# Optimization experiments

Measured on AMD Instinct MI355X. Metric: run time of the kernel, lower is better.

The kernel has to match this reference:

```python
import jax, jax.numpy as jnp
import numpy as np

B, S, DM = 2, 2048, 1024
H, HD = 16, 64  # heads, head_dims = dims // heads
SCALE = HD ** -0.5


def softmax_one(x):
    # softmax with +1 in the denominator: exp(x_i) / (1 + sum_j exp(x_j))
    # stable form: shift by m = max(max(x), 0)
    m = jnp.maximum(jnp.max(x, axis=-1, keepdims=True), 0.0)
    e = jnp.exp(x - m)
    return e / (jnp.exp(-m) + jnp.sum(e, axis=-1, keepdims=True))


def setup_inputs() -> dict:
    key = jax.random.key(0)
    ks = jax.random.split(key, 11)
    init = lambda k, shape, fan_in: jax.random.uniform(k, shape, jnp.float32, -1.0, 1.0) * (fan_in ** -0.5)
    return {
        "query": jax.random.normal(ks[0], (B, S, DM), jnp.float32),
        "key": jax.random.normal(ks[1], (B, S, DM), jnp.float32),
        "value": jax.random.normal(ks[2], (B, S, DM), jnp.float32),
        "Wq": init(ks[3], (H * HD, DM), DM), "bq": init(ks[4], (H * HD,), DM),
        "Wk": init(ks[5], (H * HD, DM), DM), "bk": init(ks[6], (H * HD,), DM),
        "Wv": init(ks[7], (H * HD, DM), DM), "bv": init(ks[8], (H * HD,), DM),
        "Wo": init(ks[9], (DM, H * HD), H * HD), "bo": init(ks[10], (DM,), H * HD),
    }


def _proj(x, W, b):
    # [B,S,DM] -> [B,H,S,HD]
    y = x @ W.T + b
    return y.reshape(B, S, H, HD).transpose(0, 2, 1, 3)


def reference(query, key, value, Wq, bq, Wk, bk, Wv, bv, Wo, bo):
    Q = _proj(query, Wq, bq)
    K = _proj(key, Wk, bk)
    V = _proj(value, Wv, bv)
    scores = jnp.einsum("bhqd,bhkd->bhqk", Q, K) * SCALE  # [B,H,S,S]
    attn = softmax_one(scores)
    out = jnp.einsum("bhqk,bhkd->bhqd", attn, V)  # [B,H,S,HD]
    out = out.transpose(0, 2, 1, 3).reshape(B, S, H * HD)
    return out @ Wo.T + bo
```

## Files before the change

### kernel.cpp

```cpp
#include <hip/hip_runtime.h>

#define B_ 2
#define S_ 2048
#define DM_ 1024
#define H_ 16
#define HD_ 64
#define QSCALE_ 0.18033688011112042f

typedef __bf16 bf16;
typedef __attribute__((ext_vector_type(4))) __bf16 bf16x4;
typedef __attribute__((ext_vector_type(8))) __bf16 bf16x8;
typedef __attribute__((ext_vector_type(4))) float f32x4;

#define MFMA16(a, b, c) __builtin_amdgcn_mfma_f32_16x16x32_bf16((a), (b), (c), 0, 0, 0)
#define EXP2(x) __builtin_amdgcn_exp2f(x)

__device__ __forceinline__ void async16(const bf16* g, bf16* l) {
  __builtin_amdgcn_global_load_lds(
      (const __attribute__((address_space(1))) void*)g,
      (__attribute__((address_space(3))) void*)l, 16, 0, 0);
}

__global__ __launch_bounds__(256) void convert_kernel(
    const float* __restrict__ q, const float* __restrict__ k,
    const float* __restrict__ v, const float* __restrict__ wq,
    const float* __restrict__ wk, const float* __restrict__ wv,
    const float* __restrict__ wo, bf16* __restrict__ dst) {
  size_t idx = ((size_t)blockIdx.x * 256 + threadIdx.x) * 8;
  const float* src;
  size_t off;
  if (idx < 4194304) { src = q; off = idx; }
  else if (idx < 8388608) { src = k; off = idx - 4194304; }
  else if (idx < 12582912) { src = v; off = idx - 8388608; }
  else if (idx < 13631488) { src = wq; off = idx - 12582912; }
  else if (idx < 14680064) { src = wk; off = idx - 13631488; }
  else if (idx < 15728640) { src = wv; off = idx - 14680064; }
  else { src = wo; off = idx - 15728640; }
  float4 a = *(const float4*)(src + off);
  float4 b = *(const float4*)(src + off + 4);
  bf16x8 o;
  o[0] = (bf16)a.x; o[1] = (bf16)a.y; o[2] = (bf16)a.z; o[3] = (bf16)a.w;
  o[4] = (bf16)b.x; o[5] = (bf16)b.y; o[6] = (bf16)b.z; o[7] = (bf16)b.w;
  *(bf16x8*)(dst + idx) = o;
}

template <int MODE>
__device__ __forceinline__ void gemm_body(const bf16* A, const bf16* W,
                                          const float* bias, bf16* C,
                                          float scale) {
  constexpr int K = 1024;
  __shared__ __align__(16) bf16 smem[128 * 136];
  bf16* As = smem;
  bf16* Bs = smem + 128 * 64;
  const int t = threadIdx.x;
  const int lane = t & 63, wave = t >> 6;
  const int quad = lane >> 4, l16 = lane & 15;
  const int m0 = blockIdx.y * 128, n0 = blockIdx.x * 128;
  const int wm = (wave >> 1) * 64, wn = (wave & 1) * 64;

  const f32x4 zero = {0.f, 0.f, 0.f, 0.f};
  f32x4 acc[4][4];
  for (int i = 0; i < 4; i++)
    for (int j = 0; j < 4; j++) acc[i][j] = zero;

  for (int k0 = 0; k0 < K; k0 += 64) {
    for (int i = 0; i < 4; ++i) {
      int c = i * 256 + t;
      int row = c >> 3, g = c & 7;
      int off = k0 + ((g ^ (row & 7)) * 8);
      async16(A + (size_t)(m0 + row) * K + off, As + c * 8);
      async16(W + (size_t)(n0 + row) * K + off, Bs + c * 8);
    }
    __syncthreads();

    for (int ks = 0; ks < 2; ks++) {
      bf16x8 af[4], bfr[4];
      for (int mb = 0; mb < 4; mb++) {
        int ra = wm + mb * 16 + l16;
        af[mb] = *(const bf16x8*)(As + ra * 64 + ((ks * 4 + quad) ^ (ra & 7)) * 8);
        int rb = wn + mb * 16 + l16;
        bfr[mb] = *(const bf16x8*)(Bs + rb * 64 + ((ks * 4 + quad) ^ (rb & 7)) * 8);
      }
      for (int mb = 0; mb < 4; mb++)
        for (int nb = 0; nb < 4; nb++)
          acc[mb][nb] = MFMA16(af[mb], bfr[nb], acc[mb][nb]);
    }
    __syncthreads();
  }

  if constexpr (MODE == 2) {
    bf16* Ct = smem;
    for (int nb = 0; nb < 4; nb++) {
      int cl = wn + nb * 16 + l16;
      float bv = bias[n0 + cl] * scale;
      for (int mb = 0; mb < 4; mb++) {
        int rowb = wm + mb * 16 + quad * 4;
        bf16x4 v;
        for (int r = 0; r < 4; r++)
          v[r] = (bf16)(acc[mb][nb][r] * scale + bv);
        *(bf16x4*)(Ct + cl * 136 + rowb) = v;
      }
    }
    __syncthreads();
    int c = t >> 1, half = t & 1;
    int colg = n0 + c;
    int hh = colg >> 6, dd = colg & 63;
    int bb = m0 >> 11, s0 = m0 & (S_ - 1);
    bf16* dst = C + (((size_t)(bb * H_ + hh)) * HD_ + dd) * S_ + s0 + half * 64;
    const bf16* srcr = Ct + c * 136 + half * 64;
    for (int j = 0; j < 8; ++j)
      *(bf16x8*)(dst + j * 8) = *(const bf16x8*)(srcr + j * 8);
  } else {
    for (int nb = 0; nb < 4; nb++) {
      int col = n0 + wn + nb * 16 + l16;
      float bv = bias[col] * scale;
      for (int mb = 0; mb < 4; mb++) {
        int rowb = m0 + wm + mb * 16 + quad * 4;
        for (int r = 0; r < 4; r++) {
          int row = rowb + r;
          float o = acc[mb][nb][r] * scale + bv;
          int bb = row >> 11, s = row & (S_ - 1);
          int h = col >> 6, d = col & 63;
          C[(((size_t)(bb * H_ + h)) * S_ + s) * HD_ + d] = (bf16)o;
        }
      }
    }
  }
}

__global__ __launch_bounds__(256, 4) void qkv_proj_kernel(
    const bf16* Xc, const float* bq, const float* bk, const float* bv,
    bf16* Qo, bf16* Ko, bf16* Vo) {
  int z = blockIdx.z;
  const bf16* A = Xc + (size_t)z * 4194304;
  const bf16* W = Xc + 12582912 + (size_t)z * 1048576;
  if (z == 0)
    gemm_body<1>(A, W, bq, Qo, QSCALE_);
  else if (z == 1)
    gemm_body<1>(A, W, bk, Ko, 1.0f);
  else
    gemm_body<2>(A, W, bv, Vo, 1.0f);
}

__global__ __launch_bounds__(256) void out_proj_kernel(const bf16* A,
                                                       const bf16* W,
                                                       const float* bias,
                                                       float* C) {
  constexpr int K = 1024, N = 1024;
  __shared__ __align__(16) bf16 As[64 * 64];
  __shared__ __align__(16) bf16 Bs[128 * 64];
  const int t = threadIdx.x;
  const int lane = t & 63, wave = t >> 6;
  const int quad = lane >> 4, l16 = lane & 15;
  const int m0 = blockIdx.y * 64, n0 = blockIdx.x * 128;

  const f32x4 zero = {0.f, 0.f, 0.f, 0.f};
  f32x4 acc[8];
  for (int i = 0; i < 8; i++) acc[i] = zero;

  for (int k0 = 0; k0 < K; k0 += 64) {
    for (int i = 0; i < 2; ++i) {
      int c = i * 256 + t;
      int row = c >> 3, g = c & 7;
      async16(A + (size_t)(m0 + row) * K + k0 + ((g ^ (row & 7)) * 8),
              As + c * 8);
    }
    for (int i = 0; i < 4; ++i) {
      int c = i * 256 + t;
      int row = c >> 3, g = c & 7;
      async16(W + (size_t)(n0 + row) * K + k0 + ((g ^ (row & 7)) * 8),
              Bs + c * 8);
    }
    __syncthreads();

    for (int ks = 0; ks < 2; ks++) {
      int ra = wave * 16 + l16;
      bf16x8 af = *(const bf16x8*)(As + ra * 64 + ((ks * 4 + quad) ^ (ra & 7)) * 8);
      for (int nb = 0; nb < 8; nb++) {
        int rb = nb * 16 + l16;
        bf16x8 bfr =
            *(const bf16x8*)(Bs + rb * 64 + ((ks * 4 + quad) ^ (rb & 7)) * 8);
        acc[nb] = MFMA16(af, bfr, acc[nb]);
      }
    }
    __syncthreads();
  }

  for (int nb = 0; nb < 8; nb++) {
    int col = n0 + nb * 16 + l16;
    float bv = bias[col];
    int rowb = m0 + wave * 16 + quad * 4;
    for (int r = 0; r < 4; r++)
      C[(size_t)(rowb + r) * N + col] = acc[nb][r] + bv;
  }
}

__global__ __launch_bounds__(256) void attn_kernel(const bf16* __restrict__ Q,
                                                   const bf16* __restrict__ Kg,
                                                   const bf16* __restrict__ VTg,
                                                   bf16* __restrict__ O) {
  __shared__ __align__(16) bf16 Ks[128 * 64];
  __shared__ __align__(16) bf16 Vt[64 * 128];
  __shared__ __align__(16) bf16 Ps[4 * 16 * 136];
  const int t = threadIdx.x;
  const int lane = t & 63, wave = t >> 6;
  const int quad = lane >> 4, l16 = lane & 15;
  const int id = blockIdx.x;
  const int bh = id & 31;
  const int q0 = (id >> 5) * 128;
  const int b = bh >> 4, h = bh & 15;
  const size_t base = ((size_t)(b * H_ + h)) * S_ * HD_;
  const bf16* Qp = Q + base;
  const bf16* Kp = Kg + base;
  const bf16* Vp = VTg + base;

  bf16x8 aq[2][2];
  for (int s = 0; s < 2; s++) {
    const bf16* qr = Qp + (size_t)(q0 + wave * 32 + s * 16 + l16) * HD_;
    aq[s][0] = *(const bf16x8*)(qr + quad * 8);
    aq[s][1] = *(const bf16x8*)(qr + 32 + quad * 8);
  }

  const f32x4 zero = {0.f, 0.f, 0.f, 0.f};
  f32x4 oc[2][4];
  for (int s = 0; s < 2; s++)
    for (int d = 0; d < 4; d++) oc[s][d] = zero;
  float rs[2] = {0.f, 0.f};

  bf16* Pw = Ps + wave * (16 * 136);

  for (int kv0 = 0; kv0 < S_; kv0 += 128) {
    for (int i = 0; i < 4; ++i) {
      int c = i * 256 + t;
      int row = c >> 3, g = c & 7;
      async16(Kp + (size_t)(kv0 + row) * HD_ + (g ^ (row & 7)) * 8, Ks + c * 8);
    }
    for (int i = 0; i < 4; ++i) {
      int c = i * 256 + t;
      int d = c >> 4, g = c & 15;
      async16(Vp + (size_t)d * S_ + kv0 + (g ^ (d & 15)) * 8, Vt + c * 8);
    }
    __syncthreads();

    f32x4 sc[2][8];
    for (int s = 0; s < 2; s++)
      for (int nb = 0; nb < 8; nb++) sc[s][nb] = zero;
    for (int ks = 0; ks < 2; ks++) {
      for (int nb = 0; nb < 8; nb++) {
        int row = nb * 16 + l16;
        int slot = (ks * 4 + quad) ^ (row & 7);
        bf16x8 kf = *(const bf16x8*)(Ks + row * 64 + slot * 8);
        sc[0][nb] = MFMA16(kf, aq[0][ks], sc[0][nb]);
        sc[1][nb] = MFMA16(kf, aq[1][ks], sc[1][nb]);
      }
    }

    for (int s = 0; s < 2; s++) {
      bf16* prow = Pw + l16 * 136 + quad * 4;
      for (int nb = 0; nb < 8; nb++) {
        float p0 = EXP2(sc[s][nb][0]);
        float p1 = EXP2(sc[s][nb][1]);
        float p2 = EXP2(sc[s][nb][2]);
        float p3 = EXP2(sc[s][nb][3]);
        rs[s] += (p0 + p1) + (p2 + p3);
        bf16x4 pv = {(bf16)p0, (bf16)p1, (bf16)p2, (bf16)p3};
        *(bf16x4*)(prow + nb * 16) = pv;
      }
      for (int ks = 0; ks < 4; ks++) {
        bf16x8 ap = *(const bf16x8*)(Pw + l16 * 136 + ks * 32 + quad * 8);
        for (int db = 0; db < 4; db++) {
          int row = db * 16 + l16;
          int slot = (ks * 4 + quad) ^ (row & 15);
          bf16x8 vf = *(const bf16x8*)(Vt + row * 128 + slot * 8);
          oc[s][db] = MFMA16(ap, vf, oc[s][db]);
        }
      }
    }
    __syncthreads();
  }

  for (int s = 0; s < 2; s++) {
    float rtot = rs[s];
    rtot += __shfl_xor(rtot, 16);
    rtot += __shfl_xor(rtot, 32);
    float l_all = 1.f + rtot;
    for (int r = 0; r < 4; r++) {
      float inv = 1.f / __shfl(l_all, quad * 4 + r);
      int qrow = q0 + wave * 32 + s * 16 + quad * 4 + r;
      size_t orow = ((size_t)(b * S_ + qrow) * H_ + h) * HD_;
      for (int db = 0; db < 4; db++)
        O[orow + db * 16 + l16] = (bf16)(oc[s][db][r] * inv);
    }
  }
}

extern "C" void kernel_launch(void* const* d_in, const int* in_sizes, int n_in,
                              void* d_out, int out_size, void* d_ws,
                              size_t ws_size, hipStream_t stream) {
  const float* query = (const float*)d_in[0];
  const float* key = (const float*)d_in[1];
  const float* value = (const float*)d_in[2];
  const float* bq = (const float*)d_in[4];
  const float* bk = (const float*)d_in[6];
  const float* bv = (const float*)d_in[8];
  const float* bo = (const float*)d_in[10];
  float* out = (float*)d_out;

  bf16* Xc = (bf16*)d_ws;
  bf16* Qw = Xc + 16777216;
  const size_t SZ = (size_t)B_ * H_ * S_ * HD_;
  bf16* Kw = Qw + SZ;
  bf16* Vw = Kw + SZ;
  bf16* Ow = Vw + SZ;

  convert_kernel<<<8192, 256, 0, stream>>>(query, key, value,
                                           (const float*)d_in[3],
                                           (const float*)d_in[5],
                                           (const float*)d_in[7],
                                           (const float*)d_in[9], Xc);
  qkv_proj_kernel<<<dim3(8, 32, 3), 256, 0, stream>>>(Xc, bq, bk, bv, Qw, Kw,
                                                      Vw);
  attn_kernel<<<512, 256, 0, stream>>>(Qw, Kw, Vw, Ow);
  out_proj_kernel<<<dim3(8, 64), 256, 0, stream>>>(Ow, Xc + 15728640, bo, out);
}
```

Measured before the change: 240.4 us.

## Split attention over two KV halves with normalize pass and narrow out-proj tiles

The attention kernel now splits the key/value range into two halves. This doubles the grid from 512 to 1024 blocks so more work is available per CU. Each half writes unnormalized fp16 partial outputs and per-row exp sums into workspace, and a new normalize kernel adds the two halves and divides by (1 + total sum). The output projection uses 64x64 tiles with a larger grid and an occupancy hint. The split costs an extra kernel launch and extra global traffic for the partial buffers, and the unnormalized fp16 partials carry some risk of precision or range loss.

```diff
diff --git a/kernel.cpp b/kernel.cpp
--- a/kernel.cpp
+++ b/kernel.cpp
@@ -8,8 +8,10 @@
 #define QSCALE_ 0.18033688011112042f
 
 typedef __bf16 bf16;
+typedef _Float16 f16;
 typedef __attribute__((ext_vector_type(4))) __bf16 bf16x4;
 typedef __attribute__((ext_vector_type(8))) __bf16 bf16x8;
+typedef __attribute__((ext_vector_type(8))) _Float16 f16x8;
 typedef __attribute__((ext_vector_type(4))) float f32x4;
 
 #define MFMA16(a, b, c) __builtin_amdgcn_mfma_f32_16x16x32_bf16((a), (b), (c), 0, 0, 0)
@@ -142,41 +144,36 @@
     gemm_body<2>(A, W, bv, Vo, 1.0f);
 }
 
-__global__ __launch_bounds__(256) void out_proj_kernel(const bf16* A,
-                                                       const bf16* W,
-                                                       const float* bias,
-                                                       float* C) {
+__global__ __launch_bounds__(256, 4) void out_proj_kernel(const bf16* A,
+                                                          const bf16* W,
+                                                          const float* bias,
+                                                          float* C) {
   constexpr int K = 1024, N = 1024;
   __shared__ __align__(16) bf16 As[64 * 64];
-  __shared__ __align__(16) bf16 Bs[128 * 64];
+  __shared__ __align__(16) bf16 Bs[64 * 64];
   const int t = threadIdx.x;
   const int lane = t & 63, wave = t >> 6;
   const int quad = lane >> 4, l16 = lane & 15;
-  const int m0 = blockIdx.y * 64, n0 = blockIdx.x * 128;
+  const int m0 = blockIdx.y * 64, n0 = blockIdx.x * 64;
 
   const f32x4 zero = {0.f, 0.f, 0.f, 0.f};
-  f32x4 acc[8];
-  for (int i = 0; i < 8; i++) acc[i] = zero;
+  f32x4 acc[4];
+  for (int i = 0; i < 4; i++) acc[i] = zero;
 
   for (int k0 = 0; k0 < K; k0 += 64) {
     for (int i = 0; i < 2; ++i) {
       int c = i * 256 + t;
       int row = c >> 3, g = c & 7;
-      async16(A + (size_t)(m0 + row) * K + k0 + ((g ^ (row & 7)) * 8),
-              As + c * 8);
-    }
-    for (int i = 0; i < 4; ++i) {
-      int c = i * 256 + t;
-      int row = c >> 3, g = c & 7;
-      async16(W + (size_t)(n0 + row) * K + k0 + ((g ^ (row & 7)) * 8),
-              Bs + c * 8);
+      int off = k0 + ((g ^ (row & 7)) * 8);
+      async16(A + (size_t)(m0 + row) * K + off, As + c * 8);
+      async16(W + (size_t)(n0 + row) * K + off, Bs + c * 8);
     }
     __syncthreads();
 
     for (int ks = 0; ks < 2; ks++) {
       int ra = wave * 16 + l16;
       bf16x8 af = *(const bf16x8*)(As + ra * 64 + ((ks * 4 + quad) ^ (ra & 7)) * 8);
-      for (int nb = 0; nb < 8; nb++) {
+      for (int nb = 0; nb < 4; nb++) {
         int rb = nb * 16 + l16;
         bf16x8 bfr =
             *(const bf16x8*)(Bs + rb * 64 + ((ks * 4 + quad) ^ (rb & 7)) * 8);
@@ -186,7 +183,7 @@
     __syncthreads();
   }
 
-  for (int nb = 0; nb < 8; nb++) {
+  for (int nb = 0; nb < 4; nb++) {
     int col = n0 + nb * 16 + l16;
     float bv = bias[col];
     int rowb = m0 + wave * 16 + quad * 4;
@@ -195,10 +192,11 @@
   }
 }
 
-__global__ __launch_bounds__(256) void attn_kernel(const bf16* __restrict__ Q,
-                                                   const bf16* __restrict__ Kg,
-                                                   const bf16* __restrict__ VTg,
-                                                   bf16* __restrict__ O) {
+__global__ __launch_bounds__(256) void attn_kernel(
+    const bf16* __restrict__ Q, const bf16* __restrict__ Kg,
+    const bf16* __restrict__ VTg, f16* __restrict__ Pa0,
+    f16* __restrict__ Pa1, float* __restrict__ rsA0,
+    float* __restrict__ rsA1) {
   __shared__ __align__(16) bf16 Ks[128 * 64];
   __shared__ __align__(16) bf16 Vt[64 * 128];
   __shared__ __align__(16) bf16 Ps[4 * 16 * 136];
@@ -207,12 +205,16 @@
   const int quad = lane >> 4, l16 = lane & 15;
   const int id = blockIdx.x;
   const int bh = id & 31;
-  const int q0 = (id >> 5) * 128;
+  const int rest = id >> 5;
+  const int split = rest & 1;
+  const int q0 = (rest >> 1) * 128;
   const int b = bh >> 4, h = bh & 15;
   const size_t base = ((size_t)(b * H_ + h)) * S_ * HD_;
   const bf16* Qp = Q + base;
   const bf16* Kp = Kg + base;
   const bf16* Vp = VTg + base;
+  f16* Pa = split ? Pa1 : Pa0;
+  float* rsA = split ? rsA1 : rsA0;
 
   bf16x8 aq[2][2];
   for (int s = 0; s < 2; s++) {
@@ -228,8 +230,9 @@
   float rs[2] = {0.f, 0.f};
 
   bf16* Pw = Ps + wave * (16 * 136);
-
-  for (int kv0 = 0; kv0 < S_; kv0 += 128) {
+  const int kvbeg = split * 1024;
+
+  for (int kv0 = kvbeg; kv0 < kvbeg + 1024; kv0 += 128) {
     for (int i = 0; i < 4; ++i) {
       int c = i * 256 + t;
       int row = c >> 3, g = c & 7;
@@ -283,15 +286,33 @@
     float rtot = rs[s];
     rtot += __shfl_xor(rtot, 16);
     rtot += __shfl_xor(rtot, 32);
-    float l_all = 1.f + rtot;
+    if (quad == 0)
+      rsA[(size_t)(b * H_ + h) * S_ + q0 + wave * 32 + s * 16 + l16] = rtot;
     for (int r = 0; r < 4; r++) {
-      float inv = 1.f / __shfl(l_all, quad * 4 + r);
       int qrow = q0 + wave * 32 + s * 16 + quad * 4 + r;
       size_t orow = ((size_t)(b * S_ + qrow) * H_ + h) * HD_;
       for (int db = 0; db < 4; db++)
-        O[orow + db * 16 + l16] = (bf16)(oc[s][db][r] * inv);
-    }
-  }
+        Pa[orow + db * 16 + l16] = (f16)(oc[s][db][r]);
+    }
+  }
+}
+
+__global__ __launch_bounds__(256) void normalize_kernel(
+    const f16* __restrict__ Pa0, const f16* __restrict__ Pa1,
+    const float* __restrict__ rs0, const float* __restrict__ rs1,
+    bf16* __restrict__ Ow) {
+  size_t flat = ((size_t)blockIdx.x * 256 + threadIdx.x) * 8;
+  int h = (int)((flat >> 6) & 15);
+  int s = (int)((flat >> 10) & 2047);
+  int b = (int)(flat >> 21);
+  int ri = (b * H_ + h) * S_ + s;
+  float inv = 1.f / (1.f + rs0[ri] + rs1[ri]);
+  f16x8 a = *(const f16x8*)(Pa0 + flat);
+  f16x8 c = *(const f16x8*)(Pa1 + flat);
+  bf16x8 o;
+  for (int j = 0; j < 8; j++)
+    o[j] = (bf16)(((float)a[j] + (float)c[j]) * inv);
+  *(bf16x8*)(Ow + flat) = o;
 }
 
 extern "C" void kernel_launch(void* const* d_in, const int* in_sizes, int n_in,
@@ -312,6 +333,10 @@
   bf16* Kw = Qw + SZ;
   bf16* Vw = Kw + SZ;
   bf16* Ow = Vw + SZ;
+  f16* Pa0 = (f16*)d_ws;
+  f16* Pa1 = Pa0 + SZ;
+  float* rs0 = (float*)((char*)d_ws + 16777216);
+  float* rs1 = rs0 + (size_t)B_ * H_ * S_;
 
   convert_kernel<<<8192, 256, 0, stream>>>(query, key, value,
                                            (const float*)d_in[3],
@@ -320,6 +345,8 @@
                                            (const float*)d_in[9], Xc);
   qkv_proj_kernel<<<dim3(8, 32, 3), 256, 0, stream>>>(Xc, bq, bk, bv, Qw, Kw,
                                                       Vw);
-  attn_kernel<<<512, 256, 0, stream>>>(Qw, Kw, Vw, Ow);
-  out_proj_kernel<<<dim3(8, 64), 256, 0, stream>>>(Ow, Xc + 15728640, bo, out);
-}
+  attn_kernel<<<1024, 256, 0, stream>>>(Qw, Kw, Vw, Pa0, Pa1, rs0, rs1);
+  normalize_kernel<<<2048, 256, 0, stream>>>(Pa0, Pa1, rs0, rs1, Ow);
+  out_proj_kernel<<<dim3(16, 64), 256, 0, stream>>>(Ow, Xc + 15728640, bo,
+                                                    out);
+}
```

Measured after the change: 244.8 us. Within noise of the previous version (+1.8%).

## Split attention KV tile across wave pairs and shrink out-proj N tile

Applied to the files above, without the earlier changes.

The attention kernel now assigns each wave 64 query rows and half of the 128-key tile, instead of 32 query rows and the full tile. K and V fragments are reused across four query sub-blocks per wave. The two key-halves' partial outputs and row sums are merged through LDS at the end. The out-projection uses 64x64 tiles, doubling the grid to improve occupancy on the small GEMM, at the cost of less B-tile reuse and an extra reduction and barrier step in attention.

```diff
diff --git a/kernel.cpp b/kernel.cpp
--- a/kernel.cpp
+++ b/kernel.cpp
@@ -142,41 +142,36 @@
     gemm_body<2>(A, W, bv, Vo, 1.0f);
 }
 
-__global__ __launch_bounds__(256) void out_proj_kernel(const bf16* A,
-                                                       const bf16* W,
-                                                       const float* bias,
-                                                       float* C) {
+__global__ __launch_bounds__(256, 4) void out_proj_kernel(const bf16* A,
+                                                          const bf16* W,
+                                                          const float* bias,
+                                                          float* C) {
   constexpr int K = 1024, N = 1024;
   __shared__ __align__(16) bf16 As[64 * 64];
-  __shared__ __align__(16) bf16 Bs[128 * 64];
+  __shared__ __align__(16) bf16 Bs[64 * 64];
   const int t = threadIdx.x;
   const int lane = t & 63, wave = t >> 6;
   const int quad = lane >> 4, l16 = lane & 15;
-  const int m0 = blockIdx.y * 64, n0 = blockIdx.x * 128;
+  const int m0 = blockIdx.y * 64, n0 = blockIdx.x * 64;
 
   const f32x4 zero = {0.f, 0.f, 0.f, 0.f};
-  f32x4 acc[8];
-  for (int i = 0; i < 8; i++) acc[i] = zero;
+  f32x4 acc[4];
+  for (int i = 0; i < 4; i++) acc[i] = zero;
 
   for (int k0 = 0; k0 < K; k0 += 64) {
     for (int i = 0; i < 2; ++i) {
       int c = i * 256 + t;
       int row = c >> 3, g = c & 7;
-      async16(A + (size_t)(m0 + row) * K + k0 + ((g ^ (row & 7)) * 8),
-              As + c * 8);
-    }
-    for (int i = 0; i < 4; ++i) {
-      int c = i * 256 + t;
-      int row = c >> 3, g = c & 7;
-      async16(W + (size_t)(n0 + row) * K + k0 + ((g ^ (row & 7)) * 8),
-              Bs + c * 8);
+      int off = k0 + ((g ^ (row & 7)) * 8);
+      async16(A + (size_t)(m0 + row) * K + off, As + c * 8);
+      async16(W + (size_t)(n0 + row) * K + off, Bs + c * 8);
     }
     __syncthreads();
 
     for (int ks = 0; ks < 2; ks++) {
       int ra = wave * 16 + l16;
       bf16x8 af = *(const bf16x8*)(As + ra * 64 + ((ks * 4 + quad) ^ (ra & 7)) * 8);
-      for (int nb = 0; nb < 8; nb++) {
+      for (int nb = 0; nb < 4; nb++) {
         int rb = nb * 16 + l16;
         bf16x8 bfr =
             *(const bf16x8*)(Bs + rb * 64 + ((ks * 4 + quad) ^ (rb & 7)) * 8);
@@ -186,7 +181,7 @@
     __syncthreads();
   }
 
-  for (int nb = 0; nb < 8; nb++) {
+  for (int nb = 0; nb < 4; nb++) {
     int col = n0 + nb * 16 + l16;
     float bv = bias[col];
     int rowb = m0 + wave * 16 + quad * 4;
@@ -195,39 +190,41 @@
   }
 }
 
-__global__ __launch_bounds__(256) void attn_kernel(const bf16* __restrict__ Q,
-                                                   const bf16* __restrict__ Kg,
-                                                   const bf16* __restrict__ VTg,
-                                                   bf16* __restrict__ O) {
+__global__ __launch_bounds__(256, 2) void attn_kernel(
+    const bf16* __restrict__ Q, const bf16* __restrict__ Kg,
+    const bf16* __restrict__ VTg, bf16* __restrict__ O) {
   __shared__ __align__(16) bf16 Ks[128 * 64];
   __shared__ __align__(16) bf16 Vt[64 * 128];
-  __shared__ __align__(16) bf16 Ps[4 * 16 * 136];
+  __shared__ __align__(16) bf16 Ps[4 * 64 * 72];
+  __shared__ float rsL[2][64];
   const int t = threadIdx.x;
   const int lane = t & 63, wave = t >> 6;
   const int quad = lane >> 4, l16 = lane & 15;
   const int id = blockIdx.x;
   const int bh = id & 31;
-  const int q0 = (id >> 5) * 128;
+  const int qt = id >> 5;
+  const int q0 = qt * 128;
   const int b = bh >> 4, h = bh & 15;
+  const int qhalf = wave >> 1, khalf = wave & 1;
   const size_t base = ((size_t)(b * H_ + h)) * S_ * HD_;
   const bf16* Qp = Q + base;
   const bf16* Kp = Kg + base;
   const bf16* Vp = VTg + base;
 
-  bf16x8 aq[2][2];
-  for (int s = 0; s < 2; s++) {
-    const bf16* qr = Qp + (size_t)(q0 + wave * 32 + s * 16 + l16) * HD_;
+  bf16x8 aq[4][2];
+  for (int s = 0; s < 4; s++) {
+    const bf16* qr = Qp + (size_t)(q0 + qhalf * 64 + s * 16 + l16) * HD_;
     aq[s][0] = *(const bf16x8*)(qr + quad * 8);
     aq[s][1] = *(const bf16x8*)(qr + 32 + quad * 8);
   }
 
   const f32x4 zero = {0.f, 0.f, 0.f, 0.f};
-  f32x4 oc[2][4];
-  for (int s = 0; s < 2; s++)
+  f32x4 oc[4][4];
+  for (int s = 0; s < 4; s++)
     for (int d = 0; d < 4; d++) oc[s][d] = zero;
-  float rs[2] = {0.f, 0.f};
-
-  bf16* Pw = Ps + wave * (16 * 136);
+  float rs[4] = {0.f, 0.f, 0.f, 0.f};
+
+  bf16* Pw = Ps + wave * (64 * 72);
 
   for (int kv0 = 0; kv0 < S_; kv0 += 128) {
     for (int i = 0; i < 4; ++i) {
@@ -242,22 +239,22 @@
     }
     __syncthreads();
 
-    f32x4 sc[2][8];
-    for (int s = 0; s < 2; s++)
-      for (int nb = 0; nb < 8; nb++) sc[s][nb] = zero;
+    f32x4 sc[4][4];
+    for (int s = 0; s < 4; s++)
+      for (int nb = 0; nb < 4; nb++) sc[s][nb] = zero;
     for (int ks = 0; ks < 2; ks++) {
-      for (int nb = 0; nb < 8; nb++) {
-        int row = nb * 16 + l16;
+      for (int nb = 0; nb < 4; nb++) {
+        int row = khalf * 64 + nb * 16 + l16;
         int slot = (ks * 4 + quad) ^ (row & 7);
         bf16x8 kf = *(const bf16x8*)(Ks + row * 64 + slot * 8);
-        sc[0][nb] = MFMA16(kf, aq[0][ks], sc[0][nb]);
-        sc[1][nb] = MFMA16(kf, aq[1][ks], sc[1][nb]);
-      }
-    }
-
-    for (int s = 0; s < 2; s++) {
-      bf16* prow = Pw + l16 * 136 + quad * 4;
-      for (int nb = 0; nb < 8; nb++) {
+        for (int s = 0; s < 4; s++)
+          sc[s][nb] = MFMA16(kf, aq[s][ks], sc[s][nb]);
+      }
+    }
+
+    for (int s = 0; s < 4; s++) {
+      bf16* prow = Pw + (s * 16 + l16) * 72 + quad * 4;
+      for (int nb = 0; nb < 4; nb++) {
         float p0 = EXP2(sc[s][nb][0]);
         float p1 = EXP2(sc[s][nb][1]);
         float p2 = EXP2(sc[s][nb][2]);
@@ -266,30 +263,56 @@
         bf16x4 pv = {(bf16)p0, (bf16)p1, (bf16)p2, (bf16)p3};
         *(bf16x4*)(prow + nb * 16) = pv;
       }
-      for (int ks = 0; ks < 4; ks++) {
-        bf16x8 ap = *(const bf16x8*)(Pw + l16 * 136 + ks * 32 + quad * 8);
+    }
+
+    for (int ks2 = 0; ks2 < 2; ks2++) {
+      bf16x8 vf[4];
+      for (int db = 0; db < 4; db++) {
+        int row = db * 16 + l16;
+        int g = khalf * 8 + ks2 * 4 + quad;
+        vf[db] = *(const bf16x8*)(Vt + row * 128 + (g ^ (row & 15)) * 8);
+      }
+      for (int s = 0; s < 4; s++) {
+        bf16x8 ap =
+            *(const bf16x8*)(Pw + (s * 16 + l16) * 72 + ks2 * 32 + quad * 8);
+        for (int db = 0; db < 4; db++)
+          oc[s][db] = MFMA16(ap, vf[db], oc[s][db]);
+      }
+    }
+    __syncthreads();
+  }
+
+  float* Ld = (float*)Ps;
+  if (khalf) {
+    for (int s = 0; s < 4; s++) {
+      float rtot = rs[s];
+      rtot += __shfl_xor(rtot, 16);
+      rtot += __shfl_xor(rtot, 32);
+      if (quad == 0) rsL[qhalf][s * 16 + l16] = rtot;
+      for (int db = 0; db < 4; db++)
+        for (int r = 0; r < 4; r++)
+          Ld[(size_t)qhalf * (64 * 68) + (s * 16 + quad * 4 + r) * 68 +
+             db * 16 + l16] = oc[s][db][r];
+    }
+  }
+  __syncthreads();
+  if (!khalf) {
+    for (int s = 0; s < 4; s++) {
+      float rtot = rs[s];
+      rtot += __shfl_xor(rtot, 16);
+      rtot += __shfl_xor(rtot, 32);
+      float l_all = 1.f + rtot + rsL[qhalf][s * 16 + l16];
+      for (int r = 0; r < 4; r++) {
+        float inv = 1.f / __shfl(l_all, quad * 4 + r);
+        int qrow = q0 + qhalf * 64 + s * 16 + quad * 4 + r;
+        size_t orow = ((size_t)(b * S_ + qrow) * H_ + h) * HD_;
         for (int db = 0; db < 4; db++) {
-          int row = db * 16 + l16;
-          int slot = (ks * 4 + quad) ^ (row & 15);
-          bf16x8 vf = *(const bf16x8*)(Vt + row * 128 + slot * 8);
-          oc[s][db] = MFMA16(ap, vf, oc[s][db]);
+          float val = oc[s][db][r] +
+                      Ld[(size_t)qhalf * (64 * 68) +
+                         (s * 16 + quad * 4 + r) * 68 + db * 16 + l16];
+          O[orow + db * 16 + l16] = (bf16)(val * inv);
         }
       }
-    }
-    __syncthreads();
-  }
-
-  for (int s = 0; s < 2; s++) {
-    float rtot = rs[s];
-    rtot += __shfl_xor(rtot, 16);
-    rtot += __shfl_xor(rtot, 32);
-    float l_all = 1.f + rtot;
-    for (int r = 0; r < 4; r++) {
-      float inv = 1.f / __shfl(l_all, quad * 4 + r);
-      int qrow = q0 + wave * 32 + s * 16 + quad * 4 + r;
-      size_t orow = ((size_t)(b * S_ + qrow) * H_ + h) * HD_;
-      for (int db = 0; db < 4; db++)
-        O[orow + db * 16 + l16] = (bf16)(oc[s][db][r] * inv);
     }
   }
 }
@@ -321,5 +344,6 @@
   qkv_proj_kernel<<<dim3(8, 32, 3), 256, 0, stream>>>(Xc, bq, bk, bv, Qw, Kw,
                                                       Vw);
   attn_kernel<<<512, 256, 0, stream>>>(Qw, Kw, Vw, Ow);
-  out_proj_kernel<<<dim3(8, 64), 256, 0, stream>>>(Ow, Xc + 15728640, bo, out);
-}
+  out_proj_kernel<<<dim3(16, 64), 256, 0, stream>>>(Ow, Xc + 15728640, bo,
+                                                    out);
+}
```

After: 222.8 us. 1.08x faster.
